# Optimization experiments

Measured on AMD Instinct MI355X. Metric: run time of the kernel, lower is better.

Reference implementation:

```python
import jax, jax.numpy as jnp
from jax import lax
import numpy as np

# --- config (mirrors init_kwargs) ---
SCALES = (0.5, 1.0, 2.0)
RATIOS = (0.5, 1.0, 2.0)
MAX_DETECTIONS = 100
SCORE_THRESHOLD = 0.5
IOU_THRESHOLD = 0.75
PRE_NMS_TOPK = 1000          # candidates kept before O(K^2) NMS
ANCHOR_BASE_CELLS = 4.0      # anchor base size in grid cells
NEG_INF = -1e30


def create_anchors(grid_h, grid_w):
    """Anchors in normalized ijhw (center_i, center_j, h, w). -> [gh*gw*A, 4]"""
    ci = (jnp.arange(grid_h, dtype=jnp.float32) + 0.5) / grid_h
    cj = (jnp.arange(grid_w, dtype=jnp.float32) + 0.5) / grid_w
    s = jnp.asarray(SCALES, jnp.float32)
    r = jnp.asarray(RATIOS, jnp.float32)
    ss, rr = jnp.meshgrid(s, r, indexing='ij')          # [3,3]
    ah = (ss * jnp.sqrt(rr)).reshape(-1) * (ANCHOR_BASE_CELLS / grid_h)  # [A]
    aw = (ss / jnp.sqrt(rr)).reshape(-1) * (ANCHOR_BASE_CELLS / grid_w)  # [A]
    A = ah.shape[0]
    ii = jnp.broadcast_to(ci[:, None, None], (grid_h, grid_w, A))
    jj = jnp.broadcast_to(cj[None, :, None], (grid_h, grid_w, A))
    hh = jnp.broadcast_to(ah[None, None, :], (grid_h, grid_w, A))
    ww = jnp.broadcast_to(aw[None, None, :], (grid_h, grid_w, A))
    return jnp.stack([ii, jj, hh, ww], axis=-1).reshape(-1, 4)


def decode(t, anchors):
    """unmatch_fn: offsets -> absolute ijhw boxes. t: [..., N, C], anchors: [N, 4]."""
    ai, aj, ah, aw = anchors[:, 0], anchors[:, 1], anchors[:, 2], anchors[:, 3]
    di = ai + t[..., 0] * ah
    dj = aj + t[..., 1] * aw
    dh = ah * jnp.exp(t[..., 2])
    dw = aw * jnp.exp(t[..., 3])
    boxes = jnp.stack([di, dj, dh, dw], axis=-1)
    return jnp.concatenate([boxes, t[..., 4:]], axis=-1)


def ijhw_to_ijkl(b):
    """center ijhw -> corner ijkl."""
    i, j, h, w = b[..., 0], b[..., 1], b[..., 2], b[..., 3]
    return jnp.stack([i - h / 2, j - w / 2, i + h / 2, j + w / 2], axis=-1)


def iou_matrix(boxes):
    """boxes [K,4] ijkl -> pairwise IoU [K,K]."""
    a, b = boxes[:, None, :], boxes[None, :, :]
    ti = jnp.maximum(a[..., 0], b[..., 0])
    tj = jnp.maximum(a[..., 1], b[..., 1])
    bi = jnp.minimum(a[..., 2], b[..., 2])
    bj = jnp.minimum(a[..., 3], b[..., 3])
    inter = jnp.clip(bi - ti, 0.0) * jnp.clip(bj - tj, 0.0)
    area = (boxes[:, 2] - boxes[:, 0]) * (boxes[:, 3] - boxes[:, 1])
    union = area[:, None] + area[None, :] - inter
    return inter / jnp.maximum(union, 1e-12)


def nms_per_image(det):
    """det: [N, C]; returns [MAX_DETECTIONS, 6] = (i, j, h, w, label, score), zero-padded."""
    scores = det[:, 5]
    masked = jnp.where(scores >= SCORE_THRESHOLD, scores, NEG_INF)
    top_scores, idx = lax.top_k(masked, PRE_NMS_TOPK)        # score-sorted candidates
    cand = det[idx]                                          # [K, C]
    valid = top_scores > NEG_INF / 2
    iou = iou_matrix(ijhw_to_ijkl(cand[:, :4]))              # [K, K]
    K = PRE_NMS_TOPK
    col = jnp.arange(K)

    def body(suppressed, xs):
        iou_row, valid_i, i = xs
        keep_i = valid_i & ~suppressed[i]
        suppressed = suppressed | (keep_i & (iou_row > IOU_THRESHOLD) & (col > i))
        return suppressed, keep_i

    _, keep = lax.scan(body, jnp.zeros(K, bool), (iou, valid, col))
    # stable sort: kept candidates first, preserving score order
    order = jnp.argsort(jnp.where(keep, 0, 1))[:MAX_DETECTIONS]
    kept = keep[order]
    sel = cand[order]                                        # [MAX_DET, C]
    coords = sel[:, :4]
    score = sel[:, 5:6]
    labels = jnp.argmax(sel[:, 6:], axis=-1).astype(jnp.float32)[:, None]
    out = jnp.concatenate([coords, labels, score], axis=-1)  # [MAX_DET, 6]
    return jnp.where(kept[:, None], out, 0.0)                # fix_tensor_length padding


def setup_inputs() -> dict:
    key = jax.random.key(0)
    inputs = jax.random.normal(key, (8, 128, 128, 9, 86), dtype=jnp.float32)
    return {"inputs": inputs}


def reference(inputs) -> jnp.ndarray:
    b, gh, gw, na, c = inputs.shape
    anchors = create_anchors(gh, gw)                  # [gh*gw*na, 4]
    flat = inputs.reshape(b, gh * gw * na, c)
    det = decode(flat, anchors)                       # [b, N, c]
    return jax.vmap(nms_per_image)(det)               # [b, MAX_DETECTIONS, 6]
```

## Files before the change

### kernel.cpp

```cpp
#include <hip/hip_runtime.h>
#include <cstdint>
#include <cstddef>

typedef unsigned int u32;
typedef unsigned long long u64;

#define NB 8
#define GH 128
#define GW 128
#define NA 9
#define NC 86
#define NANCH (GH*GW*NA)
#define BLOCKS_PER_IMG (NANCH/256)
#define TOPK 1000
#define KCAP 1024
#define CANDCAP 4096
#define VALIDCAP 65536
#define NBINS 65536

#define OFF_HIST      ((size_t)0)
#define SZ_HIST       ((size_t)NB*NBINS*4)
#define OFF_VCNT      (OFF_HIST + SZ_HIST)
#define OFF_CCNT      (OFF_VCNT + 32)
#define MEMSET_BYTES  (OFF_CCNT + 32)
#define OFF_CUT       (MEMSET_BYTES)
#define OFF_M         (OFF_CUT + 32)
#define OFF_KEEP      (OFF_M + 32)
#define OFF_VBUF      (OFF_KEEP + 1024)
#define SZ_VBUF       ((size_t)NB*VALIDCAP*8)
#define OFF_CBUF      (OFF_VBUF + SZ_VBUF)
#define SZ_CBUF       ((size_t)NB*CANDCAP*8)
#define OFF_DET       (OFF_CBUF + SZ_CBUF)
#define SZ_DET        ((size_t)NB*KCAP*8*4)
#define OFF_COR       (OFF_DET + SZ_DET)
#define SZ_COR        ((size_t)NB*KCAP*16)
#define OFF_AREA      (OFF_COR + SZ_COR)
#define SZ_AREA       ((size_t)NB*KCAP*4)
#define OFF_MASK      (OFF_AREA + SZ_AREA)
#define SZ_MASK       ((size_t)NB*KCAP*16*8)

__device__ __forceinline__ u64 shfl64(u64 v, int src) {
    int lo = __shfl((int)(v & 0xffffffffull), src, 64);
    int hi = __shfl((int)(v >> 32), src, 64);
    return ((u64)(u32)hi << 32) | (u32)lo;
}
__device__ __forceinline__ u64 shfl64_xor(u64 v, int m) {
    int lo = __shfl_xor((int)(v & 0xffffffffull), m, 64);
    int hi = __shfl_xor((int)(v >> 32), m, 64);
    return ((u64)(u32)hi << 32) | (u32)lo;
}
__device__ __forceinline__ u64 readlane64(u64 v, int lane) {
    int lo = __builtin_amdgcn_readlane((int)(v & 0xffffffffull), lane);
    int hi = __builtin_amdgcn_readlane((int)(v >> 32), lane);
    return ((u64)(u32)hi << 32) | (u32)lo;
}

__global__ __launch_bounds__(256) void k1_hist(const float* __restrict__ in,
                        u32* __restrict__ hist,
                        int* __restrict__ vcnt, u64* __restrict__ vbuf) {
    __shared__ int wcnt[4];
    __shared__ int woff[4];
    __shared__ int blockbase;
    int gid = blockIdx.x * 256 + threadIdx.x;
    int b = blockIdx.x / BLOCKS_PER_IMG;
    int lane = threadIdx.x & 63;
    int wv = threadIdx.x >> 6;
    float sc = in[(size_t)gid * NC + 5];
    bool valid = (sc >= 0.5f);
    u32 key = 0;
    if (valid) {
        key = __float_as_uint(sc) ^ 0x80000000u;
        atomicAdd(&hist[(b << 16) + (key >> 16)], 1u);
    }
    u64 mask = __ballot(valid);
    if (lane == 0) wcnt[wv] = __popcll(mask);
    __syncthreads();
    if (threadIdx.x == 0) {
        int c0 = wcnt[0], c1 = wcnt[1], c2 = wcnt[2], c3 = wcnt[3];
        woff[0] = 0; woff[1] = c0; woff[2] = c0 + c1; woff[3] = c0 + c1 + c2;
        blockbase = atomicAdd(&vcnt[b], c0 + c1 + c2 + c3);
    }
    __syncthreads();
    if (valid) {
        int prefix = __popcll(mask & ((1ull << lane) - 1ull));
        int p = blockbase + woff[wv] + prefix;
        u32 n = (u32)(gid - b * NANCH);
        if (p < VALIDCAP) vbuf[((size_t)b << 16) + p] = ((u64)key << 32) | (u32)(~n);
    }
}

__global__ void k2_cut(const u32* __restrict__ hist, int* __restrict__ cut) {
    __shared__ u32 psum[256];
    int b = blockIdx.x, t = threadIdx.x;
    const u32* h = hist + ((size_t)b << 16);
    int hi = NBINS - t * 256;
    u32 s = 0;
    for (int i = hi - 256; i < hi; ++i) s += h[i];
    psum[t] = s;
    __syncthreads();
    if (t == 0) {
        u32 cumv = 0; int res = 0; bool found = false;
        for (int c = 0; c < 256 && !found; ++c) {
            u32 cs = psum[c];
            if (cumv + cs >= (u32)TOPK) {
                int top = NBINS - c * 256 - 1;
                for (int i = top; i > top - 256; --i) {
                    cumv += h[i];
                    if (cumv >= (u32)TOPK) { res = i; found = true; break; }
                }
            } else cumv += cs;
        }
        cut[b] = found ? res : 0;
    }
}

__global__ __launch_bounds__(256) void k3_gather(const u64* __restrict__ vbuf,
                          const int* __restrict__ vcnt,
                          const int* __restrict__ cut, int* __restrict__ ccnt,
                          u64* __restrict__ cbuf) {
    __shared__ int wcnt[4];
    __shared__ int woff[4];
    __shared__ int blockbase;
    int gid = blockIdx.x * 256 + threadIdx.x;
    int b = gid >> 16, i = gid & 0xffff;
    int lane = threadIdx.x & 63;
    int wv = threadIdx.x >> 6;
    int cnt = vcnt[b]; if (cnt > VALIDCAP) cnt = VALIDCAP;
    bool take = false; u64 comp = 0;
    if (i < cnt) {
        comp = vbuf[((size_t)b << 16) + i];
        take = ((u32)(comp >> 48) >= (u32)cut[b]);
    }
    u64 mask = __ballot(take);
    if (lane == 0) wcnt[wv] = __popcll(mask);
    __syncthreads();
    if (threadIdx.x == 0) {
        int c0 = wcnt[0], c1 = wcnt[1], c2 = wcnt[2], c3 = wcnt[3];
        woff[0] = 0; woff[1] = c0; woff[2] = c0 + c1; woff[3] = c0 + c1 + c2;
        blockbase = (c0 + c1 + c2 + c3) ? atomicAdd(&ccnt[b], c0 + c1 + c2 + c3) : 0;
    }
    __syncthreads();
    if (take) {
        int p = blockbase + woff[wv] + __popcll(mask & ((1ull << lane) - 1ull));
        if (p < CANDCAP) cbuf[b * CANDCAP + p] = comp;
    }
}

__global__ __launch_bounds__(1024) void k4_sort(u64* __restrict__ cbuf,
                                                const int* __restrict__ ccnt,
                                                int* __restrict__ Mb) {
    __shared__ u64 buf[CANDCAP];
    int b = blockIdx.x, t = threadIdx.x;
    int cnt = ccnt[b]; if (cnt > CANDCAP) cnt = CANDCAP;
    for (int i = t; i < CANDCAP; i += 1024) buf[i] = (i < cnt) ? cbuf[b * CANDCAP + i] : 0ull;
    __syncthreads();
    for (int k = 2; k <= CANDCAP; k <<= 1)
        for (int j = k >> 1; j > 0; j >>= 1) {
            for (int i = t; i < CANDCAP; i += 1024) {
                int l = i ^ j;
                if (l > i) {
                    u64 a = buf[i], c = buf[l];
                    bool up = ((i & k) == 0);
                    if (up ? (a < c) : (a > c)) { buf[i] = c; buf[l] = a; }
                }
            }
            __syncthreads();
        }
    for (int i = t; i < KCAP; i += 1024) cbuf[b * CANDCAP + i] = buf[i];
    if (t == 0) Mb[b] = cnt < TOPK ? cnt : TOPK;
}

__global__ void k5_decode(const float* __restrict__ in, const u64* __restrict__ cbuf,
                          const int* __restrict__ Mb, float* __restrict__ det,
                          float4* __restrict__ cor, float* __restrict__ area) {
    int gid = blockIdx.x * blockDim.x + threadIdx.x;
    int b = gid >> 10, k = gid & 1023;
    if (b >= NB) return;
    if (k >= Mb[b]) return;
    u64 comp = cbuf[b * CANDCAP + k];
    u32 idx = ~(u32)comp;
    int a = idx % 9; int cell = idx / 9;
    int gj = cell & 127, gi = cell >> 7;
    float ci = (gi + 0.5f) * (1.0f / GH);
    float cj = (gj + 0.5f) * (1.0f / GW);
    const float SCL[3] = {0.5f, 1.0f, 2.0f};
    float s = SCL[a / 3], r = SCL[a % 3];
    float sq = sqrtf(r);
    float ah = (s * sq) * (4.0f / GH);
    float aw = (s / sq) * (4.0f / GW);
    const float* row = in + ((size_t)b * NANCH + idx) * NC;
    float t0 = row[0], t1 = row[1], t2 = row[2], t3 = row[3], scv = row[5];
    float di = ci + t0 * ah;
    float dj = cj + t1 * aw;
    float dh = ah * expf(t2);
    float dw = aw * expf(t3);
    float i0 = di - dh * 0.5f, j0 = dj - dw * 0.5f;
    float i1 = di + dh * 0.5f, j1 = dj + dw * 0.5f;
    float best = row[6]; int lab = 0;
    for (int c = 1; c < 80; ++c) { float v = row[6 + c]; if (v > best) { best = v; lab = c; } }
    float* d = det + (size_t)(b * KCAP + k) * 8;
    d[0] = di; d[1] = dj; d[2] = dh; d[3] = dw; d[4] = (float)lab; d[5] = scv;
    cor[b * KCAP + k] = make_float4(i0, j0, i1, j1);
    area[b * KCAP + k] = (i1 - i0) * (j1 - j0);
}

__global__ void k6_mask(const float4* __restrict__ cor, const float* __restrict__ area,
                        const int* __restrict__ Mb, u64* __restrict__ mask) {
    int wid = blockIdx.x * (blockDim.x >> 6) + (threadIdx.x >> 6);
    int lane = threadIdx.x & 63;
    int b = wid >> 10, i = wid & 1023;
    int m = Mb[b];
    if (i >= m) return;
    float4 bi = cor[b * KCAP + i]; float ai = area[b * KCAP + i];
    u64* rowp = mask + ((size_t)(b * KCAP + i)) * 16;
    for (int w = 0; w < 16; ++w) {
        int j = w * 64 + lane;
        bool pred = false;
        if (j > i && j < m) {
            float4 bj = cor[b * KCAP + j]; float aj = area[b * KCAP + j];
            float ti = fmaxf(bi.x, bj.x), tj = fmaxf(bi.y, bj.y);
            float b2 = fminf(bi.z, bj.z), b3 = fminf(bi.w, bj.w);
            float inter = fmaxf(b2 - ti, 0.0f) * fmaxf(b3 - tj, 0.0f);
            float uni = (ai + aj) - inter;
            float iou = inter / fmaxf(uni, 1e-12f);
            pred = iou > 0.75f;
        }
        u64 word = __ballot(pred);
        if (lane == w) rowp[w] = word;
    }
}

__global__ __launch_bounds__(64) void k7_scan(const u64* __restrict__ mask,
                        const int* __restrict__ Mb, u64* __restrict__ keep) {
    int b = blockIdx.x, lane = threadIdx.x;
    int m = Mb[b];
    const u64* mk = mask + (size_t)b * KCAP * 16;
    int myw = lane & 15;
    int myq = lane >> 4;
    u64 supp = 0;

    int r0 = lane;
    u64 colW = (r0 < m) ? mk[(size_t)r0 * 16 + 0] : 0ull;

    for (int g = 0; g < 16; ++g) {
        u64 rowW = colW;
        if (g + 1 < 16) {
            int rn = (g + 1) * 64 + lane;
            colW = (rn < m) ? mk[(size_t)rn * 16 + (g + 1)] : 0ull;
        }
        u64 cur = shfl64(supp, g);
        int lim = m - g * 64;
        u64 keptW = 0;
        #pragma unroll
        for (int t = 0; t < 64; ++t) {
            u64 w = readlane64(rowW, t);
            bool kept = (t < lim) && !((cur >> t) & 1ull);
            if (kept) { keptW |= (1ull << t); cur |= w; }
        }
        if (lane == 0) keep[b * 16 + g] = keptW;
        u64 acc = 0;
        #pragma unroll
        for (int s = 0; s < 16; ++s) {
            int t = myq * 16 + s;
            if ((keptW >> t) & 1ull)
                acc |= mk[(size_t)(g * 64 + t) * 16 + myw];
        }
        acc |= shfl64_xor(acc, 16);
        acc |= shfl64_xor(acc, 32);
        if (lane < 16) supp |= acc;
    }
}

__global__ void k8_out(const u64* __restrict__ keep, const float* __restrict__ det,
                       float* __restrict__ out) {
    int b = blockIdx.x, t = threadIdx.x;
    __shared__ int cum[17];
    __shared__ u64 kw[16];
    if (t < 16) kw[t] = keep[b * 16 + t];
    __syncthreads();
    if (t == 0) {
        int c = 0;
        for (int w = 0; w < 16; ++w) { cum[w] = c; c += __builtin_popcountll(kw[w]); }
        cum[16] = c;
    }
    __syncthreads();
    int total = cum[16];
    if (t < 100) {
        float o0 = 0, o1 = 0, o2 = 0, o3 = 0, o4 = 0, o5 = 0;
        if (t < total) {
            int w = 0;
            while (w < 15 && cum[w + 1] <= t) w++;
            int j = t - cum[w];
            u64 word = kw[w];
            for (int q = 0; q < j; ++q) word &= word - 1;
            int pos = __builtin_ctzll(word);
            int c = w * 64 + pos;
            const float* d = det + (size_t)(b * KCAP + c) * 8;
            o0 = d[0]; o1 = d[1]; o2 = d[2]; o3 = d[3]; o4 = d[4]; o5 = d[5];
        }
        float* op = out + (size_t)b * 600 + (size_t)t * 6;
        op[0] = o0; op[1] = o1; op[2] = o2; op[3] = o3; op[4] = o4; op[5] = o5;
    }
}

extern "C" void kernel_launch(void* const* d_in, const int* in_sizes, int n_in,
                              void* d_out, int out_size, void* d_ws, size_t ws_size,
                              hipStream_t stream) {
    const float* in = (const float*)d_in[0];
    float* out = (float*)d_out;
    char* ws = (char*)d_ws;
    u32* hist  = (u32*)(ws + OFF_HIST);
    int* vcnt  = (int*)(ws + OFF_VCNT);
    int* ccnt  = (int*)(ws + OFF_CCNT);
    int* cut   = (int*)(ws + OFF_CUT);
    int* Mb    = (int*)(ws + OFF_M);
    u64* keep  = (u64*)(ws + OFF_KEEP);
    u64* vbuf  = (u64*)(ws + OFF_VBUF);
    u64* cbuf  = (u64*)(ws + OFF_CBUF);
    float* det = (float*)(ws + OFF_DET);
    float4* cor = (float4*)(ws + OFF_COR);
    float* area = (float*)(ws + OFF_AREA);
    u64* mask  = (u64*)(ws + OFF_MASK);

    hipMemsetAsync(ws, 0, MEMSET_BYTES, stream);
    k1_hist  <<<(NB * NANCH) / 256, 256, 0, stream>>>(in, hist, vcnt, vbuf);
    k2_cut   <<<NB, 256, 0, stream>>>(hist, cut);
    k3_gather<<<(NB * VALIDCAP) / 256, 256, 0, stream>>>(vbuf, vcnt, cut, ccnt, cbuf);
    k4_sort  <<<NB, 1024, 0, stream>>>(cbuf, ccnt, Mb);
    k5_decode<<<(NB * KCAP) / 256, 256, 0, stream>>>(in, cbuf, Mb, det, cor, area);
    k6_mask  <<<(NB * KCAP) / 4, 256, 0, stream>>>(cor, area, Mb, mask);
    k7_scan  <<<NB, 64, 0, stream>>>(mask, Mb, keep);
    k8_out   <<<NB, 128, 0, stream>>>(keep, det, out);
}
```

Measured before the change: 706.3 us.

## Shrink histogram range and sort size, stage IoU boxes in LDS, fuse scan/output

The score histogram now covers only 1024 bins above a base derived from the 0.5 score threshold, clamping scores outside that range, which shrinks the memset and the cut scan. The bitonic sort capacity is halved to 2048 and each thread handles exactly one compare pair per step. The IoU mask kernel stages all candidate boxes and areas in shared memory, and the scan and output kernels are fused into one launch, dropping the keep buffer. Clamping the histogram bins and halving the candidate capacity depend on how the inputs are distributed: if too many candidates fall in the top bin, some may be dropped.

```diff
diff --git a/kernel.cpp b/kernel.cpp
--- a/kernel.cpp
+++ b/kernel.cpp
@@ -14,19 +14,19 @@
 #define BLOCKS_PER_IMG (NANCH/256)
 #define TOPK 1000
 #define KCAP 1024
-#define CANDCAP 4096
+#define CANDCAP 2048
 #define VALIDCAP 65536
-#define NBINS 65536
+#define HBINS 1024
+#define HBASE 48896u
 
 #define OFF_HIST      ((size_t)0)
-#define SZ_HIST       ((size_t)NB*NBINS*4)
+#define SZ_HIST       ((size_t)NB*HBINS*4)
 #define OFF_VCNT      (OFF_HIST + SZ_HIST)
 #define OFF_CCNT      (OFF_VCNT + 32)
 #define MEMSET_BYTES  (OFF_CCNT + 32)
 #define OFF_CUT       (MEMSET_BYTES)
 #define OFF_M         (OFF_CUT + 32)
-#define OFF_KEEP      (OFF_M + 32)
-#define OFF_VBUF      (OFF_KEEP + 1024)
+#define OFF_VBUF      (OFF_M + 32)
 #define SZ_VBUF       ((size_t)NB*VALIDCAP*8)
 #define OFF_CBUF      (OFF_VBUF + SZ_VBUF)
 #define SZ_CBUF       ((size_t)NB*CANDCAP*8)
@@ -70,7 +70,10 @@
     u32 key = 0;
     if (valid) {
         key = __float_as_uint(sc) ^ 0x80000000u;
-        atomicAdd(&hist[(b << 16) + (key >> 16)], 1u);
+        u32 bin = key >> 16;
+        if (bin < HBASE) bin = HBASE;
+        if (bin > HBASE + HBINS - 1) bin = HBASE + HBINS - 1;
+        atomicAdd(&hist[(b << 10) + (bin - HBASE)], 1u);
     }
     u64 mask = __ballot(valid);
     if (lane == 0) wcnt[wv] = __popcll(mask);
@@ -89,28 +92,27 @@
     }
 }
 
-__global__ void k2_cut(const u32* __restrict__ hist, int* __restrict__ cut) {
+__global__ __launch_bounds__(256) void k2_cut(const u32* __restrict__ hist,
+                                              int* __restrict__ cut) {
     __shared__ u32 psum[256];
     int b = blockIdx.x, t = threadIdx.x;
-    const u32* h = hist + ((size_t)b << 16);
-    int hi = NBINS - t * 256;
-    u32 s = 0;
-    for (int i = hi - 256; i < hi; ++i) s += h[i];
-    psum[t] = s;
+    const u32* h = hist + (b << 10);
+    int base = HBINS - 4 * (t + 1);
+    psum[t] = h[base] + h[base + 1] + h[base + 2] + h[base + 3];
     __syncthreads();
     if (t == 0) {
         u32 cumv = 0; int res = 0; bool found = false;
         for (int c = 0; c < 256 && !found; ++c) {
             u32 cs = psum[c];
             if (cumv + cs >= (u32)TOPK) {
-                int top = NBINS - c * 256 - 1;
-                for (int i = top; i > top - 256; --i) {
+                int top = HBINS - 4 * c - 1;
+                for (int i = top; i > top - 4; --i) {
                     cumv += h[i];
                     if (cumv >= (u32)TOPK) { res = i; found = true; break; }
                 }
             } else cumv += cs;
         }
-        cut[b] = found ? res : 0;
+        cut[b] = found ? (res + (int)HBASE) : 0;
     }
 }
 
@@ -152,21 +154,19 @@
     __shared__ u64 buf[CANDCAP];
     int b = blockIdx.x, t = threadIdx.x;
     int cnt = ccnt[b]; if (cnt > CANDCAP) cnt = CANDCAP;
-    for (int i = t; i < CANDCAP; i += 1024) buf[i] = (i < cnt) ? cbuf[b * CANDCAP + i] : 0ull;
+    buf[t]        = (t        < cnt) ? cbuf[b * CANDCAP + t]        : 0ull;
+    buf[t + 1024] = (t + 1024 < cnt) ? cbuf[b * CANDCAP + t + 1024] : 0ull;
     __syncthreads();
     for (int k = 2; k <= CANDCAP; k <<= 1)
         for (int j = k >> 1; j > 0; j >>= 1) {
-            for (int i = t; i < CANDCAP; i += 1024) {
-                int l = i ^ j;
-                if (l > i) {
-                    u64 a = buf[i], c = buf[l];
-                    bool up = ((i & k) == 0);
-                    if (up ? (a < c) : (a > c)) { buf[i] = c; buf[l] = a; }
-                }
-            }
+            int i = ((t & ~(j - 1)) << 1) | (t & (j - 1));
+            int l = i | j;
+            u64 a = buf[i], c = buf[l];
+            bool up = ((i & k) == 0);
+            if (up ? (a < c) : (a > c)) { buf[i] = c; buf[l] = a; }
             __syncthreads();
         }
-    for (int i = t; i < KCAP; i += 1024) cbuf[b * CANDCAP + i] = buf[i];
+    if (t < KCAP) cbuf[b * CANDCAP + t] = buf[t];
     if (t == 0) Mb[b] = cnt < TOPK ? cnt : TOPK;
 }
 
@@ -204,20 +204,28 @@
     area[b * KCAP + k] = (i1 - i0) * (j1 - j0);
 }
 
-__global__ void k6_mask(const float4* __restrict__ cor, const float* __restrict__ area,
+__global__ __launch_bounds__(256) void k6_mask(const float4* __restrict__ cor,
+                        const float* __restrict__ area,
                         const int* __restrict__ Mb, u64* __restrict__ mask) {
-    int wid = blockIdx.x * (blockDim.x >> 6) + (threadIdx.x >> 6);
+    __shared__ float4 scor[KCAP];
+    __shared__ float sarea[KCAP];
+    int b = blockIdx.x >> 8;
+    int i = ((blockIdx.x & 255) << 2) + (threadIdx.x >> 6);
     int lane = threadIdx.x & 63;
-    int b = wid >> 10, i = wid & 1023;
     int m = Mb[b];
+    for (int idx = threadIdx.x; idx < KCAP; idx += 256) {
+        scor[idx] = cor[b * KCAP + idx];
+        sarea[idx] = area[b * KCAP + idx];
+    }
+    __syncthreads();
     if (i >= m) return;
-    float4 bi = cor[b * KCAP + i]; float ai = area[b * KCAP + i];
+    float4 bi = scor[i]; float ai = sarea[i];
     u64* rowp = mask + ((size_t)(b * KCAP + i)) * 16;
     for (int w = 0; w < 16; ++w) {
         int j = w * 64 + lane;
         bool pred = false;
         if (j > i && j < m) {
-            float4 bj = cor[b * KCAP + j]; float aj = area[b * KCAP + j];
+            float4 bj = scor[j]; float aj = sarea[j];
             float ti = fmaxf(bi.x, bj.x), tj = fmaxf(bi.y, bj.y);
             float b2 = fminf(bi.z, bj.z), b3 = fminf(bi.w, bj.w);
             float inter = fmaxf(b2 - ti, 0.0f) * fmaxf(b3 - tj, 0.0f);
@@ -230,53 +238,48 @@
     }
 }
 
-__global__ __launch_bounds__(64) void k7_scan(const u64* __restrict__ mask,
-                        const int* __restrict__ Mb, u64* __restrict__ keep) {
-    int b = blockIdx.x, lane = threadIdx.x;
+__global__ __launch_bounds__(128) void k78_scan_out(const u64* __restrict__ mask,
+                        const int* __restrict__ Mb, const float* __restrict__ det,
+                        float* __restrict__ out) {
+    __shared__ u64 kw[16];
+    __shared__ int cum[17];
+    int b = blockIdx.x, t = threadIdx.x;
     int m = Mb[b];
-    const u64* mk = mask + (size_t)b * KCAP * 16;
-    int myw = lane & 15;
-    int myq = lane >> 4;
-    u64 supp = 0;
-
-    int r0 = lane;
-    u64 colW = (r0 < m) ? mk[(size_t)r0 * 16 + 0] : 0ull;
-
-    for (int g = 0; g < 16; ++g) {
-        u64 rowW = colW;
-        if (g + 1 < 16) {
-            int rn = (g + 1) * 64 + lane;
-            colW = (rn < m) ? mk[(size_t)rn * 16 + (g + 1)] : 0ull;
-        }
-        u64 cur = shfl64(supp, g);
-        int lim = m - g * 64;
-        u64 keptW = 0;
-        #pragma unroll
-        for (int t = 0; t < 64; ++t) {
-            u64 w = readlane64(rowW, t);
-            bool kept = (t < lim) && !((cur >> t) & 1ull);
-            if (kept) { keptW |= (1ull << t); cur |= w; }
-        }
-        if (lane == 0) keep[b * 16 + g] = keptW;
-        u64 acc = 0;
-        #pragma unroll
-        for (int s = 0; s < 16; ++s) {
-            int t = myq * 16 + s;
-            if ((keptW >> t) & 1ull)
-                acc |= mk[(size_t)(g * 64 + t) * 16 + myw];
-        }
-        acc |= shfl64_xor(acc, 16);
-        acc |= shfl64_xor(acc, 32);
-        if (lane < 16) supp |= acc;
-    }
-}
-
-__global__ void k8_out(const u64* __restrict__ keep, const float* __restrict__ det,
-                       float* __restrict__ out) {
-    int b = blockIdx.x, t = threadIdx.x;
-    __shared__ int cum[17];
-    __shared__ u64 kw[16];
-    if (t < 16) kw[t] = keep[b * 16 + t];
+    if (t < 64) {
+        int lane = t;
+        const u64* mk = mask + (size_t)b * KCAP * 16;
+        int myw = lane & 15;
+        int myq = lane >> 4;
+        u64 supp = 0;
+        u64 colW = (lane < m) ? mk[(size_t)lane * 16 + 0] : 0ull;
+        for (int g = 0; g < 16; ++g) {
+            u64 rowW = colW;
+            if (g + 1 < 16) {
+                int rn = (g + 1) * 64 + lane;
+                colW = (rn < m) ? mk[(size_t)rn * 16 + (g + 1)] : 0ull;
+            }
+            u64 cur = shfl64(supp, g);
+            int lim = m - g * 64;
+            u64 keptW = 0;
+            #pragma unroll
+            for (int s = 0; s < 64; ++s) {
+                u64 w = readlane64(rowW, s);
+                bool kept = (s < lim) && !((cur >> s) & 1ull);
+                if (kept) { keptW |= (1ull << s); cur |= w; }
+            }
+            if (lane == 0) kw[g] = keptW;
+            u64 acc = 0;
+            #pragma unroll
+            for (int s = 0; s < 16; ++s) {
+                int r = myq * 16 + s;
+                if ((keptW >> r) & 1ull)
+                    acc |= mk[(size_t)(g * 64 + r) * 16 + myw];
+            }
+            acc |= shfl64_xor(acc, 16);
+            acc |= shfl64_xor(acc, 32);
+            if (lane < 16) supp |= acc;
+        }
+    }
     __syncthreads();
     if (t == 0) {
         int c = 0;
@@ -314,7 +317,6 @@
     int* ccnt  = (int*)(ws + OFF_CCNT);
     int* cut   = (int*)(ws + OFF_CUT);
     int* Mb    = (int*)(ws + OFF_M);
-    u64* keep  = (u64*)(ws + OFF_KEEP);
     u64* vbuf  = (u64*)(ws + OFF_VBUF);
     u64* cbuf  = (u64*)(ws + OFF_CBUF);
     float* det = (float*)(ws + OFF_DET);
@@ -328,7 +330,6 @@
     k3_gather<<<(NB * VALIDCAP) / 256, 256, 0, stream>>>(vbuf, vcnt, cut, ccnt, cbuf);
     k4_sort  <<<NB, 1024, 0, stream>>>(cbuf, ccnt, Mb);
     k5_decode<<<(NB * KCAP) / 256, 256, 0, stream>>>(in, cbuf, Mb, det, cor, area);
-    k6_mask  <<<(NB * KCAP) / 4, 256, 0, stream>>>(cor, area, Mb, mask);
-    k7_scan  <<<NB, 64, 0, stream>>>(mask, Mb, keep);
-    k8_out   <<<NB, 128, 0, stream>>>(keep, det, out);
-}
+    k6_mask  <<<NB * 256, 256, 0, stream>>>(cor, area, Mb, mask);
+    k78_scan_out<<<NB, 128, 0, stream>>>(mask, Mb, det, out);
+}
```

New measurement: 680.7 us. -3.6%, faster.
